# Kernel optimization log

Measured on AMD Instinct MI355X. Metric: run time of the kernel, lower is better.

## Reference

```python
import jax, jax.numpy as jnp
import numpy as np

B, N, C = 8, 4096, 512

def setup_inputs() -> dict:
    key = jax.random.key(0)
    k1, k2, k3, k4, k5, k6 = jax.random.split(key, 6)
    x = jax.random.normal(k1, (B, N, C), dtype=jnp.float32)
    adj = jax.random.uniform(k2, (B, C, C), dtype=jnp.float32)
    # params: stored [in, out] so y = x @ W + b (equivalent to torch Linear)
    s = 1.0 / np.sqrt(C)
    Wqkv = jax.random.uniform(k3, (C, 3 * C), dtype=jnp.float32, minval=-s, maxval=s)
    bqkv = jax.random.uniform(k4, (3 * C,), dtype=jnp.float32, minval=-s, maxval=s)
    Wo = jax.random.uniform(k5, (C, C), dtype=jnp.float32, minval=-s, maxval=s)
    bo = jax.random.uniform(k6, (C,), dtype=jnp.float32, minval=-s, maxval=s)
    return {"x": x, "adj": adj, "Wqkv": Wqkv, "bqkv": bqkv, "Wo": Wo, "bo": bo}

def reference(x, adj, Wqkv, bqkv, Wo, bo):
    # qkv projection + ReLU gating
    qkv = jnp.einsum('bnc,cd->bnd', x, Wqkv) + bqkv          # [B,N,3C]
    q, k, v = jnp.split(qkv, 3, axis=-1)                      # each [B,N,C]
    q, k, v = jax.nn.relu(q), jax.nn.relu(k), jax.nn.relu(v)
    dk = q.shape[-1]
    # channel-wise scores: q^T k over tokens -> [B,C,C]
    scores = jnp.einsum('bnc,bnd->bcd', q, k) / jnp.sqrt(jnp.float32(dk))
    attn = jax.nn.softmax(scores, axis=-1)
    attn = attn * adj                                         # post-softmax adjacency gate
    y = jnp.einsum('bnc,bcd->bnd', v, attn)                   # value.matmul(attention)
    return jnp.einsum('bnc,cd->bnd', y, Wo) + bo
```

## Files before the change

### kernel.cpp

```cpp
#include <hip/hip_runtime.h>

#define B_ 8
#define N_ 4096
#define C_ 512

typedef _Float16 f16;
typedef __attribute__((ext_vector_type(8))) _Float16 f16x8;
typedef __attribute__((ext_vector_type(4))) _Float16 f16x4;
typedef __attribute__((ext_vector_type(4))) float f32x4;

#define GLL16(gsrc, ldst)                                                      \
  __builtin_amdgcn_global_load_lds(                                            \
      (const __attribute__((address_space(1))) void*)(gsrc),                   \
      (__attribute__((address_space(3))) void*)(ldst), 16, 0, 0)

__device__ __forceinline__ int xcd_remap(int bid, int nwg) {
  return (bid & 7) * (nwg >> 3) + (bid >> 3);
}

template <int LDA2, int LDB2, int NT>
__device__ __forceinline__ void mainloop2(const char* __restrict__ Agb,
                                          const char* __restrict__ Bgb,
                                          f16* Als, f16* Bls,
                                          f32x4 (&acc)[4][4]) {
  const int tid = threadIdx.x;
  const int lane = tid & 63;
  const int wv = tid >> 6;
  const int wr = wv >> 1;
  const int wc = wv & 1;

  const int r15 = lane & 15;
  const int kc8 = (lane >> 4) << 3;
  const int swz = (r15 & 7) << 3;
  const int k0x = kc8 ^ swz;
  const int k1x = (kc8 + 32) ^ swz;
  const int awbase = (wr * 64 + r15) * 64;
  const int bwbase = (wc * 64 + r15) * 64;

  int rowl[4], colb[4];
#pragma unroll
  for (int ld = 0; ld < 4; ++ld) {
    const int doff = (ld * 256 + tid) * 16;
    rowl[ld] = doff >> 7;
    colb[ld] = (doff & 127) ^ ((rowl[ld] & 7) << 4);
  }

  auto stage = [&](int t) {
    if (t >= NT) return;
    f16* la = Als + (t & 1) * 8192 + wv * 512;
    f16* lb = Bls + (t & 1) * 8192 + wv * 512;
#pragma unroll
    for (int ld = 0; ld < 4; ++ld) {
      GLL16(Agb + (size_t)rowl[ld] * LDA2 + (size_t)t * 128 + colb[ld],
            la + ld * 2048);
      GLL16(Bgb + (size_t)rowl[ld] * LDB2 + (size_t)t * 128 + colb[ld],
            lb + ld * 2048);
    }
  };

  stage(0);
  __syncthreads();

  for (int T = 0; T < NT; ++T) {
    stage(T + 1);
    const f16* Ab = Als + (T & 1) * 8192;
    const f16* Bb = Bls + (T & 1) * 8192;
    f16x8 af[4][2], bf[4][2];
#pragma unroll
    for (int m = 0; m < 4; ++m) {
      af[m][0] = *(const f16x8*)(Ab + awbase + m * 1024 + k0x);
      af[m][1] = *(const f16x8*)(Ab + awbase + m * 1024 + k1x);
    }
#pragma unroll
    for (int n = 0; n < 4; ++n) {
      bf[n][0] = *(const f16x8*)(Bb + bwbase + n * 1024 + k0x);
      bf[n][1] = *(const f16x8*)(Bb + bwbase + n * 1024 + k1x);
    }
#pragma unroll
    for (int s = 0; s < 2; ++s)
#pragma unroll
      for (int m = 0; m < 4; ++m)
#pragma unroll
        for (int n = 0; n < 4; ++n)
          acc[m][n] = __builtin_amdgcn_mfma_f32_16x16x32_f16(
              af[m][s], bf[n][s], acc[m][n], 0, 0, 0);
    __syncthreads();
  }
}

#define ZERO_ACC(acc)                                                          \
  f32x4 acc[4][4];                                                             \
  _Pragma("unroll") for (int zi = 0; zi < 4; ++zi)                             \
      _Pragma("unroll") for (int zj = 0; zj < 4; ++zj) {                       \
    f32x4 z = {0.f, 0.f, 0.f, 0.f};                                            \
    acc[zi][zj] = z;                                                           \
  }

__global__ void __launch_bounds__(256)
    k_prep(const float* __restrict__ x, const float* __restrict__ Wqkv,
           const float* __restrict__ Wo, f16* __restrict__ x16,
           f16* __restrict__ wqkvt, f16* __restrict__ wot) {
  const int bid = blockIdx.x;
  if (bid < 16384) {
    const int i = bid * 256 + threadIdx.x;
    float4 v = ((const float4*)x)[i];
    f16x4 h = {(f16)v.x, (f16)v.y, (f16)v.z, (f16)v.w};
    ((f16x4*)x16)[i] = h;
  } else if (bid < 19456) {
    const int idx = (bid - 16384) * 256 + threadIdx.x;
    const int n = idx >> 9, c = idx & 511;
    wqkvt[idx] = (f16)Wqkv[(size_t)c * 1536 + n];
  } else {
    const int idx = (bid - 19456) * 256 + threadIdx.x;
    const int n = idx >> 9, c = idx & 511;
    wot[idx] = (f16)Wo[(size_t)c * 512 + n];
  }
}

__global__ void __launch_bounds__(256, 2)
    k_gemm_qkv(const f16* __restrict__ x16, const f16* __restrict__ wqkvt,
               const float* __restrict__ bqkv, f16* __restrict__ q_t,
               f16* __restrict__ k_t, f16* __restrict__ v16) {
  __shared__ alignas(16) f16 Als[2 * 8192];
  __shared__ alignas(16) f16 Bls[2 * 8192];
  const int l = xcd_remap(blockIdx.x, 3072);
  const int bx = l % 12;
  const int my = l / 12;
  const char* Agb = (const char*)(x16 + (size_t)my * 128 * C_);
  const char* Bgb = (const char*)(wqkvt + (size_t)bx * 128 * C_);
  ZERO_ACC(acc);
  mainloop2<C_ * 2, C_ * 2, C_ / 64>(Agb, Bgb, Als, Bls, acc);

  const int lane = threadIdx.x & 63, wv = threadIdx.x >> 6;
  const int wr = wv >> 1, wc = wv & 1;
  const int sec = bx >> 2;
  const int colbase = bx * 128 + wc * 64;
  const int rowbase = my * 128 + wr * 64;
  const int b = rowbase >> 12;
#pragma unroll
  for (int n = 0; n < 4; ++n) {
    const int col = colbase + n * 16 + (lane & 15);
    const int cch = col & 511;
    const float bias = bqkv[col];
#pragma unroll
    for (int m = 0; m < 4; ++m) {
      const int rg = rowbase + m * 16 + ((lane >> 4) << 2);
      const int nloc = rg & 4095;
      f32x4 a = acc[m][n];
      f16x4 h = {(f16)fmaxf(a[0] + bias, 0.f), (f16)fmaxf(a[1] + bias, 0.f),
                 (f16)fmaxf(a[2] + bias, 0.f), (f16)fmaxf(a[3] + bias, 0.f)};
      if (sec == 0) {
        *(f16x4*)(q_t + ((size_t)b * C_ + cch) * N_ + nloc) = h;
      } else if (sec == 1) {
        *(f16x4*)(k_t + ((size_t)b * C_ + cch) * N_ + nloc) = h;
      } else {
        f16* dst = v16 + (size_t)rg * C_ + cch;
        dst[0] = h[0];
        dst[C_] = h[1];
        dst[2 * C_] = h[2];
        dst[3 * C_] = h[3];
      }
    }
  }
}

__global__ void __launch_bounds__(256, 2)
    k_gemm_scores(const f16* __restrict__ q_t, const f16* __restrict__ k_t,
                  f16* __restrict__ spart) {
  __shared__ alignas(16) f16 Als[2 * 8192];
  __shared__ alignas(16) f16 Bls[2 * 8192];
  const int l = xcd_remap(blockIdx.x, 512);
  const int bx = l & 3;
  const int by = (l >> 2) & 3;
  const int z = l >> 4;
  const int b = z >> 2, sp = z & 3;
  const char* Agb = (const char*)(q_t + (size_t)b * C_ * N_ +
                                  (size_t)(by * 128) * N_ + sp * 1024);
  const char* Bgb = (const char*)(k_t + (size_t)b * C_ * N_ +
                                  (size_t)(bx * 128) * N_ + sp * 1024);
  ZERO_ACC(acc);
  mainloop2<N_ * 2, N_ * 2, 16>(Agb, Bgb, Als, Bls, acc);

  const int lane = threadIdx.x & 63, wv = threadIdx.x >> 6;
  const int wr = wv >> 1, wc = wv & 1;
  f16* base = spart + (size_t)(sp * B_ + b) * C_ * C_;
#pragma unroll
  for (int n = 0; n < 4; ++n) {
    const int d = bx * 128 + wc * 64 + n * 16 + (lane & 15);
#pragma unroll
    for (int m = 0; m < 4; ++m) {
      const int c0 = by * 128 + wr * 64 + m * 16 + ((lane >> 4) << 2);
#pragma unroll
      for (int r = 0; r < 4; ++r)
        base[(size_t)(c0 + r) * C_ + d] = (f16)acc[m][n][r];
    }
  }
}

__global__ void __launch_bounds__(256)
    k_softmax_gate(const f16* __restrict__ spart,
                   const float* __restrict__ adj, f16* __restrict__ attn) {
  const int wv = threadIdx.x >> 6, lane = threadIdx.x & 63;
  const int row = blockIdx.x * 4 + wv;
  const size_t ro = (size_t)row * 512;
  const int off = lane * 8;

  float s[8] = {0.f, 0.f, 0.f, 0.f, 0.f, 0.f, 0.f, 0.f};
#pragma unroll
  for (int sp = 0; sp < 4; ++sp) {
    f16x8 v = *(const f16x8*)(spart + (size_t)sp * (B_ * C_ * C_) + ro + off);
#pragma unroll
    for (int i = 0; i < 8; ++i) s[i] += (float)v[i];
  }
  const float scale = 0.044194173824159216f;
  float mx = -1e30f;
#pragma unroll
  for (int i = 0; i < 8; ++i) {
    s[i] *= scale;
    mx = fmaxf(mx, s[i]);
  }
#pragma unroll
  for (int d = 32; d > 0; d >>= 1) mx = fmaxf(mx, __shfl_xor(mx, d, 64));
  float e[8], sum = 0.f;
#pragma unroll
  for (int i = 0; i < 8; ++i) {
    e[i] = __expf(s[i] - mx);
    sum += e[i];
  }
#pragma unroll
  for (int d = 32; d > 0; d >>= 1) sum += __shfl_xor(sum, d, 64);
  const float inv = 1.0f / sum;
  const float4 a0 = *(const float4*)(adj + ro + off);
  const float4 a1 = *(const float4*)(adj + ro + off + 4);
  f16x8 o;
  o[0] = (f16)(e[0] * inv * a0.x); o[1] = (f16)(e[1] * inv * a0.y);
  o[2] = (f16)(e[2] * inv * a0.z); o[3] = (f16)(e[3] * inv * a0.w);
  o[4] = (f16)(e[4] * inv * a1.x); o[5] = (f16)(e[5] * inv * a1.y);
  o[6] = (f16)(e[6] * inv * a1.z); o[7] = (f16)(e[7] * inv * a1.w);
  *(f16x8*)(attn + ro + off) = o;
}

__global__ void __launch_bounds__(256, 2)
    k_gemm_m(const f16* __restrict__ attn, const f16* __restrict__ wot,
             f16* __restrict__ mt) {
  __shared__ alignas(16) f16 Als[2 * 8192];
  __shared__ alignas(16) f16 Bls[2 * 8192];
  const int l = xcd_remap(blockIdx.x, 128);
  const int bx = l & 3;
  const int by = (l >> 2) & 3;
  const int b = l >> 4;
  const char* Agb = (const char*)(attn + (size_t)b * C_ * C_ +
                                  (size_t)(by * 128) * C_);
  const char* Bgb = (const char*)(wot + (size_t)(bx * 128) * C_);
  ZERO_ACC(acc);
  mainloop2<C_ * 2, C_ * 2, 8>(Agb, Bgb, Als, Bls, acc);

  const int lane = threadIdx.x & 63, wv = threadIdx.x >> 6;
  const int wr = wv >> 1, wc = wv & 1;
  f16* base = mt + (size_t)b * C_ * C_;
  const int colbase = bx * 128 + wc * 64;
  const int rowbase = by * 128 + wr * 64;
#pragma unroll
  for (int j = 0; j < 4; ++j) {
    const int e = colbase + j * 16 + (lane & 15);
#pragma unroll
    for (int i = 0; i < 4; ++i) {
      const int c0 = rowbase + i * 16 + ((lane >> 4) << 2);
      f32x4 a = acc[i][j];
      f16x4 h = {(f16)a[0], (f16)a[1], (f16)a[2], (f16)a[3]};
      *(f16x4*)(base + (size_t)e * C_ + c0) = h;
    }
  }
}

__global__ void __launch_bounds__(256, 2)
    k_gemm_out(const f16* __restrict__ v16, const f16* __restrict__ mt,
               const float* __restrict__ bo, float* __restrict__ out) {
  __shared__ alignas(16) f16 Als[2 * 8192];
  __shared__ alignas(16) f16 Bls[2 * 8192];
  const int l = xcd_remap(blockIdx.x, 1024);
  const int bx = l & 3;
  const int my = l >> 2;
  const int b = (my * 128) >> 12;
  const char* Agb = (const char*)(v16 + (size_t)my * 128 * C_);
  const char* Bgb = (const char*)(mt + (size_t)b * C_ * C_ +
                                  (size_t)(bx * 128) * C_);
  ZERO_ACC(acc);
  mainloop2<C_ * 2, C_ * 2, 8>(Agb, Bgb, Als, Bls, acc);

  const int lane = threadIdx.x & 63, wv = threadIdx.x >> 6;
  const int wr = wv >> 1, wc = wv & 1;
#pragma unroll
  for (int n = 0; n < 4; ++n) {
    const int e = bx * 128 + wc * 64 + n * 16 + (lane & 15);
    const float bias = bo[e];
#pragma unroll
    for (int m = 0; m < 4; ++m) {
      const int rg = my * 128 + wr * 64 + m * 16 + ((lane >> 4) << 2);
#pragma unroll
      for (int r = 0; r < 4; ++r)
        out[(size_t)(rg + r) * C_ + e] = acc[m][n][r] + bias;
    }
  }
}

extern "C" void kernel_launch(void* const* d_in, const int* in_sizes, int n_in,
                              void* d_out, int out_size, void* d_ws,
                              size_t ws_size, hipStream_t stream) {
  const float* x = (const float*)d_in[0];
  const float* adj = (const float*)d_in[1];
  const float* Wqkv = (const float*)d_in[2];
  const float* bqkv = (const float*)d_in[3];
  const float* Wo = (const float*)d_in[4];
  const float* bo = (const float*)d_in[5];
  float* out = (float*)d_out;

  char* ws = (char*)d_ws;
  size_t off = 0;
  auto carve = [&](size_t bytes) -> char* {
    char* p = ws + off;
    off += (bytes + 255) & ~(size_t)255;
    return p;
  };
  f16* x16 = (f16*)carve((size_t)B_ * N_ * C_ * 2);
  f16* wqkvt = (f16*)carve((size_t)3 * C_ * C_ * 2);
  f16* wot = (f16*)carve((size_t)C_ * C_ * 2);
  f16* q_t = (f16*)carve((size_t)B_ * C_ * N_ * 2);
  f16* k_t = (f16*)carve((size_t)B_ * C_ * N_ * 2);
  f16* v16 = (f16*)carve((size_t)B_ * N_ * C_ * 2);
  f16* spart = x16;
  f16* attn16 = k_t;
  f16* mt16 = q_t;

  k_prep<<<20480, 256, 0, stream>>>(x, Wqkv, Wo, x16, wqkvt, wot);
  k_gemm_qkv<<<3072, 256, 0, stream>>>(x16, wqkvt, bqkv, q_t, k_t, v16);
  k_gemm_scores<<<512, 256, 0, stream>>>(q_t, k_t, spart);
  k_softmax_gate<<<1024, 256, 0, stream>>>(spart, adj, attn16);
  k_gemm_m<<<128, 256, 0, stream>>>(attn16, wot, mt16);
  k_gemm_out<<<1024, 256, 0, stream>>>(v16, mt16, bo, out);
}
```

Before: 165.6 us.

## Make QKV and output GEMM blocks process two M-tiles with continuous pipelined mainloop

Adds a mainloop variant in which each workgroup computes two consecutive 128-row output tiles. The double-buffered K pipeline keeps running across the tile boundary, and the epilogue runs inline between them. This halves the grid for the QKV and output GEMMs and lets the next tile's loads overlap the previous epilogue, hiding prologue and tail latency. The cost is fewer workgroups, which could reduce occupancy and load balance, and longer per-block work.

Measured after the change: 170.4 us. 2.9% more time.

```diff
diff --git a/kernel.cpp b/kernel.cpp
--- a/kernel.cpp
+++ b/kernel.cpp
@@ -84,6 +84,96 @@
         for (int n = 0; n < 4; ++n)
           acc[m][n] = __builtin_amdgcn_mfma_f32_16x16x32_f16(
               af[m][s], bf[n][s], acc[m][n], 0, 0, 0);
+    __syncthreads();
+  }
+}
+
+template <int LDA2, int LDB2, int NTSUB, int MT, typename Epi>
+__device__ __forceinline__ void mainloopP(const char* __restrict__ Agb,
+                                          const char* __restrict__ Bgb,
+                                          f16* Als, f16* Bls, Epi epi) {
+  const int tid = threadIdx.x;
+  const int lane = tid & 63;
+  const int wv = tid >> 6;
+  const int wr = wv >> 1;
+  const int wc = wv & 1;
+
+  const int r15 = lane & 15;
+  const int kc8 = (lane >> 4) << 3;
+  const int swz = (r15 & 7) << 3;
+  const int k0x = kc8 ^ swz;
+  const int k1x = (kc8 + 32) ^ swz;
+  const int awbase = (wr * 64 + r15) * 64;
+  const int bwbase = (wc * 64 + r15) * 64;
+
+  int rowl[4], colb[4];
+#pragma unroll
+  for (int ld = 0; ld < 4; ++ld) {
+    const int doff = (ld * 256 + tid) * 16;
+    rowl[ld] = doff >> 7;
+    colb[ld] = (doff & 127) ^ ((rowl[ld] & 7) << 4);
+  }
+
+  f32x4 acc[4][4];
+#pragma unroll
+  for (int zi = 0; zi < 4; ++zi)
+#pragma unroll
+    for (int zj = 0; zj < 4; ++zj) {
+      f32x4 z = {0.f, 0.f, 0.f, 0.f};
+      acc[zi][zj] = z;
+    }
+
+  auto stage = [&](int t) {
+    if (t >= NTSUB * MT) return;
+    const char* Ab = Agb + (size_t)(t / NTSUB) * (128 * (size_t)LDA2) +
+                     (size_t)(t % NTSUB) * 128;
+    const char* Bb = Bgb + (size_t)(t % NTSUB) * 128;
+    f16* la = Als + (t & 1) * 8192 + wv * 512;
+    f16* lb = Bls + (t & 1) * 8192 + wv * 512;
+#pragma unroll
+    for (int ld = 0; ld < 4; ++ld) {
+      GLL16(Ab + (size_t)rowl[ld] * LDA2 + colb[ld], la + ld * 2048);
+      GLL16(Bb + (size_t)rowl[ld] * LDB2 + colb[ld], lb + ld * 2048);
+    }
+  };
+
+  stage(0);
+  __syncthreads();
+
+#pragma unroll
+  for (int T = 0; T < NTSUB * MT; ++T) {
+    stage(T + 1);
+    const f16* Ab = Als + (T & 1) * 8192;
+    const f16* Bb = Bls + (T & 1) * 8192;
+    f16x8 af[4][2], bf[4][2];
+#pragma unroll
+    for (int m = 0; m < 4; ++m) {
+      af[m][0] = *(const f16x8*)(Ab + awbase + m * 1024 + k0x);
+      af[m][1] = *(const f16x8*)(Ab + awbase + m * 1024 + k1x);
+    }
+#pragma unroll
+    for (int n = 0; n < 4; ++n) {
+      bf[n][0] = *(const f16x8*)(Bb + bwbase + n * 1024 + k0x);
+      bf[n][1] = *(const f16x8*)(Bb + bwbase + n * 1024 + k1x);
+    }
+#pragma unroll
+    for (int s = 0; s < 2; ++s)
+#pragma unroll
+      for (int m = 0; m < 4; ++m)
+#pragma unroll
+        for (int n = 0; n < 4; ++n)
+          acc[m][n] = __builtin_amdgcn_mfma_f32_16x16x32_f16(
+              af[m][s], bf[n][s], acc[m][n], 0, 0, 0);
+    if (((T + 1) % NTSUB) == 0) {
+      epi(T / NTSUB, acc);
+#pragma unroll
+      for (int zi = 0; zi < 4; ++zi)
+#pragma unroll
+        for (int zj = 0; zj < 4; ++zj) {
+          f32x4 z = {0.f, 0.f, 0.f, 0.f};
+          acc[zi][zj] = z;
+        }
+    }
     __syncthreads();
   }
 }
@@ -123,45 +213,47 @@
                f16* __restrict__ k_t, f16* __restrict__ v16) {
   __shared__ alignas(16) f16 Als[2 * 8192];
   __shared__ alignas(16) f16 Bls[2 * 8192];
-  const int l = xcd_remap(blockIdx.x, 3072);
+  const int l = xcd_remap(blockIdx.x, 1536);
   const int bx = l % 12;
-  const int my = l / 12;
-  const char* Agb = (const char*)(x16 + (size_t)my * 128 * C_);
+  const int pj = l / 12;
+  const char* Agb = (const char*)(x16 + (size_t)pj * 256 * C_);
   const char* Bgb = (const char*)(wqkvt + (size_t)bx * 128 * C_);
-  ZERO_ACC(acc);
-  mainloop2<C_ * 2, C_ * 2, C_ / 64>(Agb, Bgb, Als, Bls, acc);
 
   const int lane = threadIdx.x & 63, wv = threadIdx.x >> 6;
   const int wr = wv >> 1, wc = wv & 1;
   const int sec = bx >> 2;
   const int colbase = bx * 128 + wc * 64;
-  const int rowbase = my * 128 + wr * 64;
-  const int b = rowbase >> 12;
-#pragma unroll
-  for (int n = 0; n < 4; ++n) {
-    const int col = colbase + n * 16 + (lane & 15);
-    const int cch = col & 511;
-    const float bias = bqkv[col];
-#pragma unroll
-    for (int m = 0; m < 4; ++m) {
-      const int rg = rowbase + m * 16 + ((lane >> 4) << 2);
-      const int nloc = rg & 4095;
-      f32x4 a = acc[m][n];
-      f16x4 h = {(f16)fmaxf(a[0] + bias, 0.f), (f16)fmaxf(a[1] + bias, 0.f),
-                 (f16)fmaxf(a[2] + bias, 0.f), (f16)fmaxf(a[3] + bias, 0.f)};
-      if (sec == 0) {
-        *(f16x4*)(q_t + ((size_t)b * C_ + cch) * N_ + nloc) = h;
-      } else if (sec == 1) {
-        *(f16x4*)(k_t + ((size_t)b * C_ + cch) * N_ + nloc) = h;
-      } else {
-        f16* dst = v16 + (size_t)rg * C_ + cch;
-        dst[0] = h[0];
-        dst[C_] = h[1];
-        dst[2 * C_] = h[2];
-        dst[3 * C_] = h[3];
+
+  auto epi = [&](int g, f32x4 (&acc)[4][4]) {
+    const int rowbase = pj * 256 + g * 128 + wr * 64;
+    const int b = rowbase >> 12;
+#pragma unroll
+    for (int n = 0; n < 4; ++n) {
+      const int col = colbase + n * 16 + (lane & 15);
+      const int cch = col & 511;
+      const float bias = bqkv[col];
+#pragma unroll
+      for (int m = 0; m < 4; ++m) {
+        const int rg = rowbase + m * 16 + ((lane >> 4) << 2);
+        const int nloc = rg & 4095;
+        f32x4 a = acc[m][n];
+        f16x4 h = {(f16)fmaxf(a[0] + bias, 0.f), (f16)fmaxf(a[1] + bias, 0.f),
+                   (f16)fmaxf(a[2] + bias, 0.f), (f16)fmaxf(a[3] + bias, 0.f)};
+        if (sec == 0) {
+          *(f16x4*)(q_t + ((size_t)b * C_ + cch) * N_ + nloc) = h;
+        } else if (sec == 1) {
+          *(f16x4*)(k_t + ((size_t)b * C_ + cch) * N_ + nloc) = h;
+        } else {
+          f16* dst = v16 + (size_t)rg * C_ + cch;
+          dst[0] = h[0];
+          dst[C_] = h[1];
+          dst[2 * C_] = h[2];
+          dst[3 * C_] = h[3];
+        }
       }
     }
-  }
+  };
+  mainloopP<C_ * 2, C_ * 2, 8, 2>(Agb, Bgb, Als, Bls, epi);
 }
 
 __global__ void __launch_bounds__(256, 2)
@@ -278,30 +370,32 @@
                const float* __restrict__ bo, float* __restrict__ out) {
   __shared__ alignas(16) f16 Als[2 * 8192];
   __shared__ alignas(16) f16 Bls[2 * 8192];
-  const int l = xcd_remap(blockIdx.x, 1024);
+  const int l = xcd_remap(blockIdx.x, 512);
   const int bx = l & 3;
-  const int my = l >> 2;
-  const int b = (my * 128) >> 12;
-  const char* Agb = (const char*)(v16 + (size_t)my * 128 * C_);
+  const int pj = l >> 2;
+  const int b = pj >> 4;
+  const char* Agb = (const char*)(v16 + (size_t)pj * 256 * C_);
   const char* Bgb = (const char*)(mt + (size_t)b * C_ * C_ +
                                   (size_t)(bx * 128) * C_);
-  ZERO_ACC(acc);
-  mainloop2<C_ * 2, C_ * 2, 8>(Agb, Bgb, Als, Bls, acc);
-
   const int lane = threadIdx.x & 63, wv = threadIdx.x >> 6;
   const int wr = wv >> 1, wc = wv & 1;
-#pragma unroll
-  for (int n = 0; n < 4; ++n) {
-    const int e = bx * 128 + wc * 64 + n * 16 + (lane & 15);
-    const float bias = bo[e];
-#pragma unroll
-    for (int m = 0; m < 4; ++m) {
-      const int rg = my * 128 + wr * 64 + m * 16 + ((lane >> 4) << 2);
-#pragma unroll
-      for (int r = 0; r < 4; ++r)
-        out[(size_t)(rg + r) * C_ + e] = acc[m][n][r] + bias;
-    }
-  }
+
+  auto epi = [&](int g, f32x4 (&acc)[4][4]) {
+#pragma unroll
+    for (int n = 0; n < 4; ++n) {
+      const int e = bx * 128 + wc * 64 + n * 16 + (lane & 15);
+      const float bias = bo[e];
+#pragma unroll
+      for (int m = 0; m < 4; ++m) {
+        const int rg = pj * 256 + g * 128 + wr * 64 + m * 16 +
+                       ((lane >> 4) << 2);
+#pragma unroll
+        for (int r = 0; r < 4; ++r)
+          out[(size_t)(rg + r) * C_ + e] = acc[m][n][r] + bias;
+      }
+    }
+  };
+  mainloopP<C_ * 2, C_ * 2, 8, 2>(Agb, Bgb, Als, Bls, epi);
 }
 
 extern "C" void kernel_launch(void* const* d_in, const int* in_sizes, int n_in,
@@ -333,9 +427,9 @@
   f16* mt16 = q_t;
 
   k_prep<<<20480, 256, 0, stream>>>(x, Wqkv, Wo, x16, wqkvt, wot);
-  k_gemm_qkv<<<3072, 256, 0, stream>>>(x16, wqkvt, bqkv, q_t, k_t, v16);
+  k_gemm_qkv<<<1536, 256, 0, stream>>>(x16, wqkvt, bqkv, q_t, k_t, v16);
   k_gemm_scores<<<512, 256, 0, stream>>>(q_t, k_t, spart);
   k_softmax_gate<<<1024, 256, 0, stream>>>(spart, adj, attn16);
   k_gemm_m<<<128, 256, 0, stream>>>(attn16, wot, mt16);
-  k_gemm_out<<<1024, 256, 0, stream>>>(v16, mt16, bo, out);
-}
+  k_gemm_out<<<512, 256, 0, stream>>>(v16, mt16, bo, out);
+}
```
